# Performance work log

Measured on AMD Instinct MI355X. Metric: run time of the kernel, lower is better.

The kernel has to match this reference:

```python
import jax, jax.numpy as jnp
import numpy as np

N, E, H = 100000, 1250000, 64
NF, EF = 16, 3
BN_EPS = 1e-5
HALF = H // 2


def setup_inputs() -> dict:
    key = jax.random.key(0)
    ks = jax.random.split(key, 24)
    g = lambda i, shape, s=0.05: jax.random.normal(ks[i], shape, dtype=jnp.float32) * s
    return {
        "x": jax.random.normal(ks[0], (N, NF), dtype=jnp.float32),
        "edge_attr": jax.random.normal(ks[1], (E, EF), dtype=jnp.float32),
        "edge_index": jax.random.randint(ks[2], (2, E), 0, N),
        "W_node": g(3, (NF, H)), "b_node": g(4, (H,)),
        "W_edge": g(5, (EF, H)), "b_edge": g(6, (H,)),
        "W_lin0": g(7, (H, H)), "b_lin0": g(8, (H,)),
        "W_att0": g(9, (2 * H + EF, 1)), "b_att0": g(10, (1,)),
        "W_sage_l": g(11, (H, H)), "b_sage_l": g(12, (H,)),
        "W_sage_r": g(13, (H, H)),
        "W_gcn": g(14, (H, H)), "b_gcn": g(15, (H,)),
        "bn_gamma": jnp.ones((3, H), jnp.float32),
        "bn_beta": jnp.zeros((3, H), jnp.float32),
        "W_r1": g(16, (H, H)), "b_r1": g(17, (H,)),
        "W_r2": g(18, (H, HALF)), "b_r2": g(19, (HALF,)),
        "W_r3": g(20, (HALF, 1)), "b_r3": g(21, (1,)),
    }


def _bn_eval(x, gamma, beta):
    # eval-mode BatchNorm1d with running_mean=0, running_var=1
    return x * (gamma / jnp.sqrt(1.0 + BN_EPS)) + beta


def _edge_att(h, src, dst, edge_attr, W, b, Wa, ba):
    # EdgeAttentionLayer: lin -> per-edge attention MLP -> scatter-add at dst
    h = h @ W + b                                   # [N,H]
    hi, hj = h[dst], h[src]                         # [E,H] gathers
    a = jnp.concatenate([hi, hj, edge_attr], -1) @ Wa + ba   # [E,1]
    a = jax.nn.sigmoid(jax.nn.leaky_relu(a, 0.01))
    return jax.ops.segment_sum(hj * a, dst, num_segments=N)


def _sage(h, src, dst, Wl, bl, Wr):
    # SAGEConv (mean aggregation): lin_l(mean_j x_j) + lin_r(x)
    agg = jax.ops.segment_sum(h[src], dst, num_segments=N)
    cnt = jax.ops.segment_sum(jnp.ones((src.shape[0], 1), h.dtype), dst, num_segments=N)
    mean = agg / jnp.maximum(cnt, 1.0)
    return mean @ Wl + bl + h @ Wr


def _gcn(h, src, dst, W, b):
    # GCNConv with self-loops and symmetric normalization
    hw = h @ W
    loop = jnp.arange(N)
    s = jnp.concatenate([src, loop])
    d = jnp.concatenate([dst, loop])
    deg = jax.ops.segment_sum(jnp.ones(s.shape[0], hw.dtype), d, num_segments=N)
    dis = jnp.where(deg > 0, jax.lax.rsqrt(jnp.maximum(deg, 1.0)), 0.0)
    norm = dis[s] * dis[d]                          # [E+N]
    return jax.ops.segment_sum(hw[s] * norm[:, None], d, num_segments=N) + b


def reference(x, edge_attr, edge_index, W_node, b_node, W_edge, b_edge,
              W_lin0, b_lin0, W_att0, b_att0, W_sage_l, b_sage_l, W_sage_r,
              W_gcn, b_gcn, bn_gamma, bn_beta, W_r1, b_r1, W_r2, b_r2, W_r3, b_r3):
    src, dst = edge_index[0], edge_index[1]
    h = x @ W_node + b_node
    _unused = edge_attr @ W_edge + b_edge  # computed in original forward, never used

    # layer 0: EdgeAttentionLayer + BN + ReLU (+residual; eval dropout = identity)
    ident = h
    h = _edge_att(h, src, dst, edge_attr, W_lin0, b_lin0, W_att0, b_att0)
    h = jax.nn.relu(_bn_eval(h, bn_gamma[0], bn_beta[0])) + ident

    # layer 1: SAGEConv
    ident = h
    h = _sage(h, src, dst, W_sage_l, b_sage_l, W_sage_r)
    h = jax.nn.relu(_bn_eval(h, bn_gamma[1], bn_beta[1])) + ident

    # layer 2: GCNConv
    ident = h
    h = _gcn(h, src, dst, W_gcn, b_gcn)
    h = jax.nn.relu(_bn_eval(h, bn_gamma[2], bn_beta[2])) + ident

    h = jax.nn.relu(h @ W_r1 + b_r1)
    h = jax.nn.relu(h @ W_r2 + b_r2)
    return h @ W_r3 + b_r3  # [N,1]
```

## Files before the change

### kernel.cpp

```cpp
#include <hip/hip_runtime.h>
#include <hip/hip_fp16.h>
#include <math.h>

#define NODES 100000
#define EDGES 1250000
#define HD 64
#define NFD 16
#define CHUNK 1024
#define NCHUNK ((NODES + CHUNK - 1) / CHUNK)
#define BN_INV 0.9999950000374996f
#define LP 65


__global__ void k_hist(const int* __restrict__ ei, int* __restrict__ deg) {
  int e = blockIdx.x * blockDim.x + threadIdx.x;
  if (e < EDGES) atomicAdd(&deg[ei[EDGES + e]], 1);
}

__global__ void k_scan1(const int* __restrict__ deg, int* __restrict__ part) {
  __shared__ int lds[256];
  int t = threadIdx.x, b = blockIdx.x;
  int base = b * CHUNK + t * 4;
  int s = 0;
#pragma unroll
  for (int m = 0; m < 4; m++) { int i = base + m; if (i < NODES) s += deg[i]; }
  lds[t] = s; __syncthreads();
  for (int off = 128; off > 0; off >>= 1) {
    if (t < off) lds[t] += lds[t + off];
    __syncthreads();
  }
  if (t == 0) part[b] = lds[0];
}

__global__ void k_scan2(int* __restrict__ part) {
  if (threadIdx.x == 0 && blockIdx.x == 0) {
    int run = 0;
    for (int c = 0; c < NCHUNK; c++) { int v = part[c]; part[c] = run; run += v; }
  }
}

__global__ void k_scan3(const int* __restrict__ deg, const int* __restrict__ part,
                        int* __restrict__ rowptr, int* __restrict__ cur,
                        float* __restrict__ dis) {
  __shared__ int lds[256];
  int t = threadIdx.x, b = blockIdx.x;
  int base = b * CHUNK + t * 4;
  int dl[4]; int s = 0;
#pragma unroll
  for (int m = 0; m < 4; m++) { int i = base + m; dl[m] = (i < NODES) ? deg[i] : 0; s += dl[m]; }
  lds[t] = s; __syncthreads();
  for (int off = 1; off < 256; off <<= 1) {
    int add = (t >= off) ? lds[t - off] : 0;
    __syncthreads();
    lds[t] += add;
    __syncthreads();
  }
  int run = part[b] + lds[t] - s;
#pragma unroll
  for (int m = 0; m < 4; m++) {
    int i = base + m;
    if (i < NODES) {
      rowptr[i] = run; cur[i] = run;
      dis[i] = 1.0f / sqrtf((float)(dl[m] + 1));
    }
    run += dl[m];
  }
  if (b == 0 && t == 0) rowptr[NODES] = EDGES;
}

__global__ void k_fillatt(const int* __restrict__ ei, const float* __restrict__ ea,
                          const float* __restrict__ cvec, const float* __restrict__ dvec,
                          const float* __restrict__ Wa, const float* __restrict__ ba,
                          int* __restrict__ cur, float2* __restrict__ sa) {
  int e = blockIdx.x * blockDim.x + threadIdx.x;
  if (e >= EDGES) return;
  int s = ei[e], d = ei[EDGES + e];
  float alin = cvec[d] + dvec[s] + ea[3 * e] * Wa[128] + ea[3 * e + 1] * Wa[129] +
               ea[3 * e + 2] * Wa[130] + ba[0];
  float lr = alin >= 0.f ? alin : 0.01f * alin;
  float a = 1.f / (1.f + expf(-lr));
  int p = atomicAdd(&cur[d], 1);
  sa[p] = make_float2(__int_as_float(s), a);
}


__device__ __forceinline__ void store16h(__half* dst, const float* v) {
  uint u[8];
#pragma unroll
  for (int j = 0; j < 8; j++) {
    __half2 h = __float22half2_rn(make_float2(v[2 * j], v[2 * j + 1]));
    u[j] = *reinterpret_cast<uint*>(&h);
  }
  uint4* o = (uint4*)dst;
  o[0] = make_uint4(u[0], u[1], u[2], u[3]);
  o[1] = make_uint4(u[4], u[5], u[6], u[7]);
}

#define AGG_BODY16(TABLE, WEXPR0, WEXPR1, WEXPR2, WEXPR3)                        \
  float4 acc0 = make_float4(0.f, 0.f, 0.f, 0.f);                                 \
  float4 acc1 = make_float4(0.f, 0.f, 0.f, 0.f);                                 \
  float4 acc2 = make_float4(0.f, 0.f, 0.f, 0.f);                                 \
  float4 acc3 = make_float4(0.f, 0.f, 0.f, 0.f);                                 \
  int last = end - 1;                                                            \
  for (int m = start; m < end; m += 16) {                                        \
    int e0 = m + sub, e1 = e0 + 4, e2 = e0 + 8, e3 = e0 + 12;                    \
    float2 s0 = sa[min(e0, last)], s1 = sa[min(e1, last)];                       \
    float2 s2 = sa[min(e2, last)], s3 = sa[min(e3, last)];                       \
    float w0 = (e0 < end) ? (WEXPR0) : 0.f;                                      \
    float w1 = (e1 < end) ? (WEXPR1) : 0.f;                                      \
    float w2 = (e2 < end) ? (WEXPR2) : 0.f;                                      \
    float w3 = (e3 < end) ? (WEXPR3) : 0.f;                                      \
    uint2 u0 = *((const uint2*)(TABLE + (size_t)__float_as_int(s0.x) * HD) + col); \
    uint2 u1 = *((const uint2*)(TABLE + (size_t)__float_as_int(s1.x) * HD) + col); \
    uint2 u2 = *((const uint2*)(TABLE + (size_t)__float_as_int(s2.x) * HD) + col); \
    uint2 u3 = *((const uint2*)(TABLE + (size_t)__float_as_int(s3.x) * HD) + col); \
    {                                                                            \
      float2 fa = __half22float2(*reinterpret_cast<__half2*>(&u0.x));            \
      float2 fb = __half22float2(*reinterpret_cast<__half2*>(&u0.y));            \
      acc0.x = fmaf(w0, fa.x, acc0.x); acc0.y = fmaf(w0, fa.y, acc0.y);          \
      acc0.z = fmaf(w0, fb.x, acc0.z); acc0.w = fmaf(w0, fb.y, acc0.w);          \
    }                                                                            \
    {                                                                            \
      float2 fa = __half22float2(*reinterpret_cast<__half2*>(&u1.x));            \
      float2 fb = __half22float2(*reinterpret_cast<__half2*>(&u1.y));            \
      acc1.x = fmaf(w1, fa.x, acc1.x); acc1.y = fmaf(w1, fa.y, acc1.y);          \
      acc1.z = fmaf(w1, fb.x, acc1.z); acc1.w = fmaf(w1, fb.y, acc1.w);          \
    }                                                                            \
    {                                                                            \
      float2 fa = __half22float2(*reinterpret_cast<__half2*>(&u2.x));            \
      float2 fb = __half22float2(*reinterpret_cast<__half2*>(&u2.y));            \
      acc2.x = fmaf(w2, fa.x, acc2.x); acc2.y = fmaf(w2, fa.y, acc2.y);          \
      acc2.z = fmaf(w2, fb.x, acc2.z); acc2.w = fmaf(w2, fb.y, acc2.w);          \
    }                                                                            \
    {                                                                            \
      float2 fa = __half22float2(*reinterpret_cast<__half2*>(&u3.x));            \
      float2 fb = __half22float2(*reinterpret_cast<__half2*>(&u3.y));            \
      acc3.x = fmaf(w3, fa.x, acc3.x); acc3.y = fmaf(w3, fa.y, acc3.y);          \
      acc3.z = fmaf(w3, fb.x, acc3.z); acc3.w = fmaf(w3, fb.y, acc3.w);          \
    }                                                                            \
  }                                                                              \
  acc0.x = (acc0.x + acc1.x) + (acc2.x + acc3.x);                                \
  acc0.y = (acc0.y + acc1.y) + (acc2.y + acc3.y);                                \
  acc0.z = (acc0.z + acc1.z) + (acc2.z + acc3.z);                                \
  acc0.w = (acc0.w + acc1.w) + (acc2.w + acc3.w);                                \
  _Pragma("unroll")                                                              \
  for (int off = 16; off <= 32; off <<= 1) {                                     \
    acc0.x += __shfl_xor(acc0.x, off); acc0.y += __shfl_xor(acc0.y, off);        \
    acc0.z += __shfl_xor(acc0.z, off); acc0.w += __shfl_xor(acc0.w, off);        \
  }


__global__ __launch_bounds__(256) void k_lin0(
    const float* __restrict__ x,
    const float* __restrict__ Wn, const float* __restrict__ bn,
    const float* __restrict__ Wl, const float* __restrict__ bl,
    const float* __restrict__ Wa,
    float* __restrict__ hA, __half* __restrict__ hB16,
    float* __restrict__ cvec, float* __restrict__ dvec) {
  __shared__ float sh[64 * LP];
  __shared__ float sc[4][64], sd[4][64];
  int slot = threadIdx.x & 63;
  int cc = __builtin_amdgcn_readfirstlane(threadIdx.x >> 6);
  int c0 = cc * 16;
  int n0 = blockIdx.x * 64 + slot;
  bool valid = n0 < NODES;
  int n = valid ? n0 : NODES - 1;
  const float4* xr = (const float4*)(x + (size_t)n * NFD);
  float acc[16];
#pragma unroll
  for (int j = 0; j < 16; j++) acc[j] = bn[c0 + j];
#pragma unroll
  for (int q = 0; q < 4; q++) {
    float4 xa = xr[q];
    float xs[4] = {xa.x, xa.y, xa.z, xa.w};
#pragma unroll
    for (int t = 0; t < 4; t++)
#pragma unroll
      for (int j = 0; j < 16; j++)
        acc[j] = fmaf(xs[t], Wn[(q * 4 + t) * HD + c0 + j], acc[j]);
  }
#pragma unroll
  for (int j = 0; j < 16; j++) sh[slot * LP + c0 + j] = acc[j];
  if (valid) {
    float4* o = (float4*)(hA + (size_t)n * HD + c0);
    o[0] = make_float4(acc[0], acc[1], acc[2], acc[3]);
    o[1] = make_float4(acc[4], acc[5], acc[6], acc[7]);
    o[2] = make_float4(acc[8], acc[9], acc[10], acc[11]);
    o[3] = make_float4(acc[12], acc[13], acc[14], acc[15]);
  }
  __syncthreads();
  float a2[16];
#pragma unroll
  for (int j = 0; j < 16; j++) a2[j] = bl[c0 + j];
#pragma unroll 8
  for (int k = 0; k < 64; k++) {
    float hk = sh[slot * LP + k];
#pragma unroll
    for (int j = 0; j < 16; j++)
      a2[j] = fmaf(hk, Wl[k * HD + c0 + j], a2[j]);
  }
  float cn = 0.f, dn = 0.f;
#pragma unroll
  for (int j = 0; j < 16; j++) {
    cn = fmaf(a2[j], Wa[c0 + j], cn);
    dn = fmaf(a2[j], Wa[64 + c0 + j], dn);
  }
  if (valid) store16h(hB16 + (size_t)n * HD + c0, a2);
  sc[cc][slot] = cn;
  sd[cc][slot] = dn;
  __syncthreads();
  if (cc == 0 && valid) {
    cvec[n] = sc[0][slot] + sc[1][slot] + sc[2][slot] + sc[3][slot];
    dvec[n] = sd[0][slot] + sd[1][slot] + sd[2][slot] + sd[3][slot];
  }
}

__global__ __launch_bounds__(256) void k_agg_att(
    const float2* __restrict__ sa, const int* __restrict__ rowptr,
    const float* __restrict__ hA, const __half* __restrict__ hB16,
    const float* __restrict__ g, const float* __restrict__ bt,
    float* __restrict__ hC, __half* __restrict__ hC16) {
  int lane = threadIdx.x & 63;
  int node = __builtin_amdgcn_readfirstlane(blockIdx.x * 4 + (threadIdx.x >> 6));
  if (node >= NODES) return;
  int start = rowptr[node], end = rowptr[node + 1];
  int sub = lane >> 4, col = lane & 15;
  float4 gg = ((const float4*)g)[col];
  float4 bb = ((const float4*)bt)[col];
  float4 ha = *((const float4*)(hA + (size_t)node * HD) + col);
  AGG_BODY16(hB16, s0.y, s1.y, s2.y, s3.y)
  if (lane < 16) {
    float4 v;
    v.x = fmaxf(acc0.x * (gg.x * BN_INV) + bb.x, 0.f) + ha.x;
    v.y = fmaxf(acc0.y * (gg.y * BN_INV) + bb.y, 0.f) + ha.y;
    v.z = fmaxf(acc0.z * (gg.z * BN_INV) + bb.z, 0.f) + ha.z;
    v.w = fmaxf(acc0.w * (gg.w * BN_INV) + bb.w, 0.f) + ha.w;
    *((float4*)(hC + (size_t)node * HD) + col) = v;
    __half2 p0 = __float22half2_rn(make_float2(v.x, v.y));
    __half2 p1 = __float22half2_rn(make_float2(v.z, v.w));
    uint2 u;
    u.x = *reinterpret_cast<uint*>(&p0);
    u.y = *reinterpret_cast<uint*>(&p1);
    *((uint2*)(hC16 + (size_t)node * HD) + col) = u;
  }
}

__global__ __launch_bounds__(256) void k_msage(
    const float2* __restrict__ sa, const int* __restrict__ rowptr,
    const float* __restrict__ hC, const __half* __restrict__ hC16,
    const float* __restrict__ Wl, const float* __restrict__ bl,
    const float* __restrict__ Wr, const float* __restrict__ Wg,
    const float* __restrict__ g, const float* __restrict__ bt,
    const float* __restrict__ dis,
    float* __restrict__ hA, float* __restrict__ hD, __half* __restrict__ hD16) {
  __shared__ float sh[64 * LP];
  int lane = threadIdx.x & 63;
  int wu = __builtin_amdgcn_readfirstlane(threadIdx.x >> 6);
  int sub = lane >> 4, col = lane & 15;
  int nbase = blockIdx.x * 64;
  for (int i = 0; i < 16; i++) {
    int slot = wu * 16 + i;
    int nn = min(nbase + slot, NODES - 1);
    int start = rowptr[nn], end = rowptr[nn + 1];
    float rdeg = 1.f / fmaxf((float)(end - start), 1.f);
    AGG_BODY16(hC16, 1.f, 1.f, 1.f, 1.f)
    if (lane < 16) {
      sh[slot * LP + col * 4 + 0] = acc0.x * rdeg;
      sh[slot * LP + col * 4 + 1] = acc0.y * rdeg;
      sh[slot * LP + col * 4 + 2] = acc0.z * rdeg;
      sh[slot * LP + col * 4 + 3] = acc0.w * rdeg;
    }
  }
  __syncthreads();
  int c0 = wu * 16;
  int n0 = nbase + lane;
  bool valid = n0 < NODES;
  int n = valid ? n0 : NODES - 1;
  const float4* cr = (const float4*)(hC + (size_t)n * HD);
  float acc[16];
#pragma unroll
  for (int j = 0; j < 16; j++) acc[j] = bl[c0 + j];
#pragma unroll 8
  for (int k = 0; k < 64; k++) {
    float mk = sh[lane * LP + k];
#pragma unroll
    for (int j = 0; j < 16; j++)
      acc[j] = fmaf(mk, Wl[k * HD + c0 + j], acc[j]);
  }
#pragma unroll 4
  for (int q = 0; q < 16; q++) {
    float4 ac = cr[q];
    float cs[4] = {ac.x, ac.y, ac.z, ac.w};
#pragma unroll
    for (int t = 0; t < 4; t++)
#pragma unroll
      for (int j = 0; j < 16; j++)
        acc[j] = fmaf(cs[t], Wr[(q * 4 + t) * HD + c0 + j], acc[j]);
  }
  float tv[16];
  {
    float4 r0 = cr[wu * 4 + 0], r1 = cr[wu * 4 + 1], r2 = cr[wu * 4 + 2], r3 = cr[wu * 4 + 3];
    float rv[16] = {r0.x, r0.y, r0.z, r0.w, r1.x, r1.y, r1.z, r1.w,
                    r2.x, r2.y, r2.z, r2.w, r3.x, r3.y, r3.z, r3.w};
#pragma unroll
    for (int j = 0; j < 16; j++)
      tv[j] = fmaxf(acc[j] * (g[c0 + j] * BN_INV) + bt[c0 + j], 0.f) + rv[j];
  }
  __syncthreads();
#pragma unroll
  for (int j = 0; j < 16; j++) sh[lane * LP + c0 + j] = tv[j];
  if (valid) {
    float4* o = (float4*)(hA + (size_t)n * HD + c0);
    o[0] = make_float4(tv[0], tv[1], tv[2], tv[3]);
    o[1] = make_float4(tv[4], tv[5], tv[6], tv[7]);
    o[2] = make_float4(tv[8], tv[9], tv[10], tv[11]);
    o[3] = make_float4(tv[12], tv[13], tv[14], tv[15]);
  }
  __syncthreads();
  float di = dis[n];
  float a2[16];
#pragma unroll
  for (int j = 0; j < 16; j++) a2[j] = 0.f;
#pragma unroll 8
  for (int k = 0; k < 64; k++) {
    float tk = sh[lane * LP + k];
#pragma unroll
    for (int j = 0; j < 16; j++)
      a2[j] = fmaf(tk, Wg[k * HD + c0 + j], a2[j]);
  }
#pragma unroll
  for (int j = 0; j < 16; j++) a2[j] *= di;
  if (valid) {
    float4* o = (float4*)(hD + (size_t)n * HD + c0);
    o[0] = make_float4(a2[0], a2[1], a2[2], a2[3]);
    o[1] = make_float4(a2[4], a2[5], a2[6], a2[7]);
    o[2] = make_float4(a2[8], a2[9], a2[10], a2[11]);
    o[3] = make_float4(a2[12], a2[13], a2[14], a2[15]);
    store16h(hD16 + (size_t)n * HD + c0, a2);
  }
}

__global__ __launch_bounds__(256) void k_gcnreg(
    const float2* __restrict__ sa, const int* __restrict__ rowptr,
    const float* __restrict__ dis,
    const float* __restrict__ hA,
    const float* __restrict__ hD,
    const __half* __restrict__ hD16,
    const float* __restrict__ bg,
    const float* __restrict__ g, const float* __restrict__ bt,
    const float* __restrict__ W1, const float* __restrict__ b1,
    const float* __restrict__ W2, const float* __restrict__ b2,
    const float* __restrict__ W3, const float* __restrict__ b3,
    float* __restrict__ out) {
  __shared__ float sh[64 * LP];
  __shared__ float sred[4][64];
  int lane = threadIdx.x & 63;
  int wu = __builtin_amdgcn_readfirstlane(threadIdx.x >> 6);
  int sub = lane >> 4, col = lane & 15;
  int nbase = blockIdx.x * 64;
  float4 gg = ((const float4*)g)[col];
  float4 bb = ((const float4*)bt)[col];
  float4 bgv = ((const float4*)bg)[col];
  for (int i = 0; i < 16; i++) {
    int slot = wu * 16 + i;
    int nn = min(nbase + slot, NODES - 1);
    int start = rowptr[nn], end = rowptr[nn + 1];
    float di = dis[nn];
    float4 sv = *((const float4*)(hD + (size_t)nn * HD) + col);
    float4 ha = *((const float4*)(hA + (size_t)nn * HD) + col);
    AGG_BODY16(hD16, 1.f, 1.f, 1.f, 1.f)
    if (lane < 16) {
      sh[slot * LP + col * 4 + 0] =
          fmaxf((di * (acc0.x + sv.x) + bgv.x) * (gg.x * BN_INV) + bb.x, 0.f) + ha.x;
      sh[slot * LP + col * 4 + 1] =
          fmaxf((di * (acc0.y + sv.y) + bgv.y) * (gg.y * BN_INV) + bb.y, 0.f) + ha.y;
      sh[slot * LP + col * 4 + 2] =
          fmaxf((di * (acc0.z + sv.z) + bgv.z) * (gg.z * BN_INV) + bb.z, 0.f) + ha.z;
      sh[slot * LP + col * 4 + 3] =
          fmaxf((di * (acc0.w + sv.w) + bgv.w) * (gg.w * BN_INV) + bb.w, 0.f) + ha.w;
    }
  }
  __syncthreads();
  int c0 = wu * 16;
  int n0 = nbase + lane;
  bool valid = n0 < NODES;
  int n = valid ? n0 : NODES - 1;
  float acc[16];
#pragma unroll
  for (int j = 0; j < 16; j++) acc[j] = b1[c0 + j];
#pragma unroll 8
  for (int k = 0; k < 64; k++) {
    float rk = sh[lane * LP + k];
#pragma unroll
    for (int j = 0; j < 16; j++)
      acc[j] = fmaf(rk, W1[k * HD + c0 + j], acc[j]);
  }
  float t1v[16];
#pragma unroll
  for (int j = 0; j < 16; j++) t1v[j] = fmaxf(acc[j], 0.f);
  __syncthreads();
#pragma unroll
  for (int j = 0; j < 16; j++) sh[lane * LP + c0 + j] = t1v[j];
  __syncthreads();
  int d0 = wu * 8;
  float a2[8];
#pragma unroll
  for (int j = 0; j < 8; j++) a2[j] = b2[d0 + j];
#pragma unroll 8
  for (int k = 0; k < 64; k++) {
    float tk = sh[lane * LP + k];
#pragma unroll
    for (int j = 0; j < 8; j++)
      a2[j] = fmaf(tk, W2[k * 32 + d0 + j], a2[j]);
  }
  float part = 0.f;
#pragma unroll
  for (int j = 0; j < 8; j++) part = fmaf(fmaxf(a2[j], 0.f), W3[d0 + j], part);
  sred[wu][lane] = part;
  __syncthreads();
  if (wu == 0 && valid)
    out[n] = sred[0][lane] + sred[1][lane] + sred[2][lane] + sred[3][lane] + b3[0];
}


extern "C" void kernel_launch(void* const* d_in, const int* in_sizes, int n_in,
                              void* d_out, int out_size, void* d_ws, size_t ws_size,
                              hipStream_t stream) {
  const float* x      = (const float*)d_in[0];
  const float* ea     = (const float*)d_in[1];
  const int*   ei     = (const int*)d_in[2];
  const float* W_node = (const float*)d_in[3];
  const float* b_node = (const float*)d_in[4];
  const float* W_lin0 = (const float*)d_in[7];
  const float* b_lin0 = (const float*)d_in[8];
  const float* W_att0 = (const float*)d_in[9];
  const float* b_att0 = (const float*)d_in[10];
  const float* W_sl   = (const float*)d_in[11];
  const float* b_sl   = (const float*)d_in[12];
  const float* W_sr   = (const float*)d_in[13];
  const float* W_gcn  = (const float*)d_in[14];
  const float* b_gcn  = (const float*)d_in[15];
  const float* bn_g   = (const float*)d_in[16];
  const float* bn_b   = (const float*)d_in[17];
  const float* W_r1   = (const float*)d_in[18];
  const float* b_r1   = (const float*)d_in[19];
  const float* W_r2   = (const float*)d_in[20];
  const float* b_r2   = (const float*)d_in[21];
  const float* W_r3   = (const float*)d_in[22];
  const float* b_r3   = (const float*)d_in[23];
  float* out = (float*)d_out;

  char* ws = (char*)d_ws;
  size_t o = 0;
  auto alloc = [&](size_t bytes) -> void* {
    void* p = ws + o;
    o += (bytes + 255) & ~(size_t)255;
    return p;
  };
  int*    deg    = (int*)alloc(NODES * 4);
  int*    rowptr = (int*)alloc((NODES + 1) * 4);
  int*    cur    = (int*)alloc(NODES * 4);
  int*    part   = (int*)alloc(256 * 4);
  float2* sa     = (float2*)alloc((size_t)EDGES * 8);
  float*  hA     = (float*)alloc((size_t)NODES * HD * 4);
  float*  hC     = (float*)alloc((size_t)NODES * HD * 4);
  float*  hD     = (float*)alloc((size_t)NODES * HD * 4);
  __half* hB16   = (__half*)alloc((size_t)NODES * HD * 2);
  __half* hC16   = (__half*)alloc((size_t)NODES * HD * 2);
  __half* hD16   = (__half*)alloc((size_t)NODES * HD * 2);
  float*  cvec   = (float*)alloc(NODES * 4);
  float*  dvec   = (float*)alloc(NODES * 4);
  float*  dis    = (float*)alloc(NODES * 4);
  (void)ws_size; (void)in_sizes; (void)n_in; (void)out_size;

  const int EB  = (EDGES + 255) / 256;
  const int NT  = (NODES + 63) / 64;
  const int NBW = (NODES + 3) / 4;

  hipMemsetAsync(deg, 0, NODES * 4, stream);
  k_hist<<<EB, 256, 0, stream>>>(ei, deg);
  k_scan1<<<NCHUNK, 256, 0, stream>>>(deg, part);
  k_scan2<<<1, 64, 0, stream>>>(part);
  k_scan3<<<NCHUNK, 256, 0, stream>>>(deg, part, rowptr, cur, dis);

  k_lin0<<<NT, 256, 0, stream>>>(x, W_node, b_node, W_lin0, b_lin0, W_att0,
                                 hA, hB16, cvec, dvec);
  k_fillatt<<<EB, 256, 0, stream>>>(ei, ea, cvec, dvec, W_att0, b_att0, cur, sa);
  k_agg_att<<<NBW, 256, 0, stream>>>(sa, rowptr, hA, hB16,
                                     bn_g + 0 * HD, bn_b + 0 * HD, hC, hC16);
  k_msage<<<NT, 256, 0, stream>>>(sa, rowptr, hC, hC16, W_sl, b_sl, W_sr, W_gcn,
                                  bn_g + 1 * HD, bn_b + 1 * HD, dis, hA, hD, hD16);
  k_gcnreg<<<NT, 256, 0, stream>>>(sa, rowptr, dis, hA, hD, hD16, b_gcn,
                                   bn_g + 2 * HD, bn_b + 2 * HD,
                                   W_r1, b_r1, W_r2, b_r2, W_r3, b_r3, out);
}
```

Before: 341.3 us.

## Use 8 waves per block and interleave two-node gathers in SAGE/GCN kernels

The fused SAGE and GCN+regressor kernels go from 256 to 512 threads per block, so each wave aggregates 8 nodes instead of 16 and computes 8 instead of 16 output columns in the dense stages. Inside the aggregation loop each wave now walks two nodes' neighbor lists together, issuing both sets of gathers per iteration to raise memory-level parallelism. The macro body is moved into inline helper functions. The cost is more registers for the paired accumulators and wasted iterations when the two nodes' degrees differ.

Result: slower. 351.7 us (+3.0%).

```diff
diff --git a/kernel.cpp b/kernel.cpp
--- a/kernel.cpp
+++ b/kernel.cpp
@@ -96,58 +96,81 @@
   o[1] = make_uint4(u[4], u[5], u[6], u[7]);
 }
 
-#define AGG_BODY16(TABLE, WEXPR0, WEXPR1, WEXPR2, WEXPR3)                        \
+__device__ __forceinline__ void store8h(__half* dst, const float* v) {
+  uint u[4];
+#pragma unroll
+  for (int j = 0; j < 4; j++) {
+    __half2 h = __float22half2_rn(make_float2(v[2 * j], v[2 * j + 1]));
+    u[j] = *reinterpret_cast<uint*>(&h);
+  }
+  *(uint4*)dst = make_uint4(u[0], u[1], u[2], u[3]);
+}
+
+__device__ __forceinline__ void gstep(const __half* __restrict__ tab,
+                                      const float2* __restrict__ sa,
+                                      int m, int end, int last, int sub, int col,
+                                      bool weighted,
+                                      float4& A0, float4& A1, float4& A2, float4& A3) {
+  int e0 = m + sub, e1 = e0 + 4, e2 = e0 + 8, e3 = e0 + 12;
+  float2 s0 = sa[min(e0, last)], s1 = sa[min(e1, last)];
+  float2 s2 = sa[min(e2, last)], s3 = sa[min(e3, last)];
+  float w0 = (e0 < end) ? (weighted ? s0.y : 1.f) : 0.f;
+  float w1 = (e1 < end) ? (weighted ? s1.y : 1.f) : 0.f;
+  float w2 = (e2 < end) ? (weighted ? s2.y : 1.f) : 0.f;
+  float w3 = (e3 < end) ? (weighted ? s3.y : 1.f) : 0.f;
+  uint2 u0 = *((const uint2*)(tab + (size_t)__float_as_int(s0.x) * HD) + col);
+  uint2 u1 = *((const uint2*)(tab + (size_t)__float_as_int(s1.x) * HD) + col);
+  uint2 u2 = *((const uint2*)(tab + (size_t)__float_as_int(s2.x) * HD) + col);
+  uint2 u3 = *((const uint2*)(tab + (size_t)__float_as_int(s3.x) * HD) + col);
+  {
+    float2 fa = __half22float2(*reinterpret_cast<__half2*>(&u0.x));
+    float2 fb = __half22float2(*reinterpret_cast<__half2*>(&u0.y));
+    A0.x = fmaf(w0, fa.x, A0.x); A0.y = fmaf(w0, fa.y, A0.y);
+    A0.z = fmaf(w0, fb.x, A0.z); A0.w = fmaf(w0, fb.y, A0.w);
+  }
+  {
+    float2 fa = __half22float2(*reinterpret_cast<__half2*>(&u1.x));
+    float2 fb = __half22float2(*reinterpret_cast<__half2*>(&u1.y));
+    A1.x = fmaf(w1, fa.x, A1.x); A1.y = fmaf(w1, fa.y, A1.y);
+    A1.z = fmaf(w1, fb.x, A1.z); A1.w = fmaf(w1, fb.y, A1.w);
+  }
+  {
+    float2 fa = __half22float2(*reinterpret_cast<__half2*>(&u2.x));
+    float2 fb = __half22float2(*reinterpret_cast<__half2*>(&u2.y));
+    A2.x = fmaf(w2, fa.x, A2.x); A2.y = fmaf(w2, fa.y, A2.y);
+    A2.z = fmaf(w2, fb.x, A2.z); A2.w = fmaf(w2, fb.y, A2.w);
+  }
+  {
+    float2 fa = __half22float2(*reinterpret_cast<__half2*>(&u3.x));
+    float2 fb = __half22float2(*reinterpret_cast<__half2*>(&u3.y));
+    A3.x = fmaf(w3, fa.x, A3.x); A3.y = fmaf(w3, fa.y, A3.y);
+    A3.z = fmaf(w3, fb.x, A3.z); A3.w = fmaf(w3, fb.y, A3.w);
+  }
+}
+
+__device__ __forceinline__ float4 red4(float4 a0, float4 a1, float4 a2, float4 a3) {
+  float4 r;
+  r.x = (a0.x + a1.x) + (a2.x + a3.x);
+  r.y = (a0.y + a1.y) + (a2.y + a3.y);
+  r.z = (a0.z + a1.z) + (a2.z + a3.z);
+  r.w = (a0.w + a1.w) + (a2.w + a3.w);
+#pragma unroll
+  for (int off = 16; off <= 32; off <<= 1) {
+    r.x += __shfl_xor(r.x, off); r.y += __shfl_xor(r.y, off);
+    r.z += __shfl_xor(r.z, off); r.w += __shfl_xor(r.w, off);
+  }
+  return r;
+}
+
+#define AGG_BODY16(TABLE, WEIGHTED)                                              \
   float4 acc0 = make_float4(0.f, 0.f, 0.f, 0.f);                                 \
   float4 acc1 = make_float4(0.f, 0.f, 0.f, 0.f);                                 \
   float4 acc2 = make_float4(0.f, 0.f, 0.f, 0.f);                                 \
   float4 acc3 = make_float4(0.f, 0.f, 0.f, 0.f);                                 \
   int last = end - 1;                                                            \
-  for (int m = start; m < end; m += 16) {                                        \
-    int e0 = m + sub, e1 = e0 + 4, e2 = e0 + 8, e3 = e0 + 12;                    \
-    float2 s0 = sa[min(e0, last)], s1 = sa[min(e1, last)];                       \
-    float2 s2 = sa[min(e2, last)], s3 = sa[min(e3, last)];                       \
-    float w0 = (e0 < end) ? (WEXPR0) : 0.f;                                      \
-    float w1 = (e1 < end) ? (WEXPR1) : 0.f;                                      \
-    float w2 = (e2 < end) ? (WEXPR2) : 0.f;                                      \
-    float w3 = (e3 < end) ? (WEXPR3) : 0.f;                                      \
-    uint2 u0 = *((const uint2*)(TABLE + (size_t)__float_as_int(s0.x) * HD) + col); \
-    uint2 u1 = *((const uint2*)(TABLE + (size_t)__float_as_int(s1.x) * HD) + col); \
-    uint2 u2 = *((const uint2*)(TABLE + (size_t)__float_as_int(s2.x) * HD) + col); \
-    uint2 u3 = *((const uint2*)(TABLE + (size_t)__float_as_int(s3.x) * HD) + col); \
-    {                                                                            \
-      float2 fa = __half22float2(*reinterpret_cast<__half2*>(&u0.x));            \
-      float2 fb = __half22float2(*reinterpret_cast<__half2*>(&u0.y));            \
-      acc0.x = fmaf(w0, fa.x, acc0.x); acc0.y = fmaf(w0, fa.y, acc0.y);          \
-      acc0.z = fmaf(w0, fb.x, acc0.z); acc0.w = fmaf(w0, fb.y, acc0.w);          \
-    }                                                                            \
-    {                                                                            \
-      float2 fa = __half22float2(*reinterpret_cast<__half2*>(&u1.x));            \
-      float2 fb = __half22float2(*reinterpret_cast<__half2*>(&u1.y));            \
-      acc1.x = fmaf(w1, fa.x, acc1.x); acc1.y = fmaf(w1, fa.y, acc1.y);          \
-      acc1.z = fmaf(w1, fb.x, acc1.z); acc1.w = fmaf(w1, fb.y, acc1.w);          \
-    }                                                                            \
-    {                                                                            \
-      float2 fa = __half22float2(*reinterpret_cast<__half2*>(&u2.x));            \
-      float2 fb = __half22float2(*reinterpret_cast<__half2*>(&u2.y));            \
-      acc2.x = fmaf(w2, fa.x, acc2.x); acc2.y = fmaf(w2, fa.y, acc2.y);          \
-      acc2.z = fmaf(w2, fb.x, acc2.z); acc2.w = fmaf(w2, fb.y, acc2.w);          \
-    }                                                                            \
-    {                                                                            \
-      float2 fa = __half22float2(*reinterpret_cast<__half2*>(&u3.x));            \
-      float2 fb = __half22float2(*reinterpret_cast<__half2*>(&u3.y));            \
-      acc3.x = fmaf(w3, fa.x, acc3.x); acc3.y = fmaf(w3, fa.y, acc3.y);          \
-      acc3.z = fmaf(w3, fb.x, acc3.z); acc3.w = fmaf(w3, fb.y, acc3.w);          \
-    }                                                                            \
-  }                                                                              \
-  acc0.x = (acc0.x + acc1.x) + (acc2.x + acc3.x);                                \
-  acc0.y = (acc0.y + acc1.y) + (acc2.y + acc3.y);                                \
-  acc0.z = (acc0.z + acc1.z) + (acc2.z + acc3.z);                                \
-  acc0.w = (acc0.w + acc1.w) + (acc2.w + acc3.w);                                \
-  _Pragma("unroll")                                                              \
-  for (int off = 16; off <= 32; off <<= 1) {                                     \
-    acc0.x += __shfl_xor(acc0.x, off); acc0.y += __shfl_xor(acc0.y, off);        \
-    acc0.z += __shfl_xor(acc0.z, off); acc0.w += __shfl_xor(acc0.w, off);        \
-  }
+  for (int m = start; m < end; m += 16)                                          \
+    gstep(TABLE, sa, m, end, last, sub, col, WEIGHTED, acc0, acc1, acc2, acc3);  \
+  float4 accr = red4(acc0, acc1, acc2, acc3);
 
 
 __global__ __launch_bounds__(256) void k_lin0(
@@ -228,13 +251,13 @@
   float4 gg = ((const float4*)g)[col];
   float4 bb = ((const float4*)bt)[col];
   float4 ha = *((const float4*)(hA + (size_t)node * HD) + col);
-  AGG_BODY16(hB16, s0.y, s1.y, s2.y, s3.y)
+  AGG_BODY16(hB16, true)
   if (lane < 16) {
     float4 v;
-    v.x = fmaxf(acc0.x * (gg.x * BN_INV) + bb.x, 0.f) + ha.x;
-    v.y = fmaxf(acc0.y * (gg.y * BN_INV) + bb.y, 0.f) + ha.y;
-    v.z = fmaxf(acc0.z * (gg.z * BN_INV) + bb.z, 0.f) + ha.z;
-    v.w = fmaxf(acc0.w * (gg.w * BN_INV) + bb.w, 0.f) + ha.w;
+    v.x = fmaxf(accr.x * (gg.x * BN_INV) + bb.x, 0.f) + ha.x;
+    v.y = fmaxf(accr.y * (gg.y * BN_INV) + bb.y, 0.f) + ha.y;
+    v.z = fmaxf(accr.z * (gg.z * BN_INV) + bb.z, 0.f) + ha.z;
+    v.w = fmaxf(accr.w * (gg.w * BN_INV) + bb.w, 0.f) + ha.w;
     *((float4*)(hC + (size_t)node * HD) + col) = v;
     __half2 p0 = __float22half2_rn(make_float2(v.x, v.y));
     __half2 p1 = __float22half2_rn(make_float2(v.z, v.w));
@@ -245,7 +268,7 @@
   }
 }
 
-__global__ __launch_bounds__(256) void k_msage(
+__global__ __launch_bounds__(512) void k_msage(
     const float2* __restrict__ sa, const int* __restrict__ rowptr,
     const float* __restrict__ hC, const __half* __restrict__ hC16,
     const float* __restrict__ Wl, const float* __restrict__ bl,
@@ -258,33 +281,52 @@
   int wu = __builtin_amdgcn_readfirstlane(threadIdx.x >> 6);
   int sub = lane >> 4, col = lane & 15;
   int nbase = blockIdx.x * 64;
-  for (int i = 0; i < 16; i++) {
-    int slot = wu * 16 + i;
-    int nn = min(nbase + slot, NODES - 1);
-    int start = rowptr[nn], end = rowptr[nn + 1];
-    float rdeg = 1.f / fmaxf((float)(end - start), 1.f);
-    AGG_BODY16(hC16, 1.f, 1.f, 1.f, 1.f)
+  for (int i = 0; i < 8; i += 2) {
+    int slotA = wu * 8 + i, slotB = slotA + 1;
+    int nA = min(nbase + slotA, NODES - 1);
+    int nB = min(nbase + slotB, NODES - 1);
+    int sA = rowptr[nA], eA = rowptr[nA + 1];
+    int sB = rowptr[nB], eB = rowptr[nB + 1];
+    int lenA = eA - sA, lenB = eB - sB;
+    int lastA = (lenA > 0) ? eA - 1 : 0;
+    int lastB = (lenB > 0) ? eB - 1 : 0;
+    float rdA = 1.f / fmaxf((float)lenA, 1.f);
+    float rdB = 1.f / fmaxf((float)lenB, 1.f);
+    float4 A0 = make_float4(0, 0, 0, 0), A1 = A0, A2 = A0, A3 = A0;
+    float4 B0 = A0, B1 = A0, B2 = A0, B3 = A0;
+    int iters = (max(lenA, lenB) + 15) >> 4;
+    int mA = sA, mB = sB;
+    for (int it = 0; it < iters; ++it, mA += 16, mB += 16) {
+      gstep(hC16, sa, mA, eA, lastA, sub, col, false, A0, A1, A2, A3);
+      gstep(hC16, sa, mB, eB, lastB, sub, col, false, B0, B1, B2, B3);
+    }
+    float4 ra = red4(A0, A1, A2, A3);
+    float4 rb = red4(B0, B1, B2, B3);
     if (lane < 16) {
-      sh[slot * LP + col * 4 + 0] = acc0.x * rdeg;
-      sh[slot * LP + col * 4 + 1] = acc0.y * rdeg;
-      sh[slot * LP + col * 4 + 2] = acc0.z * rdeg;
-      sh[slot * LP + col * 4 + 3] = acc0.w * rdeg;
+      sh[slotA * LP + col * 4 + 0] = ra.x * rdA;
+      sh[slotA * LP + col * 4 + 1] = ra.y * rdA;
+      sh[slotA * LP + col * 4 + 2] = ra.z * rdA;
+      sh[slotA * LP + col * 4 + 3] = ra.w * rdA;
+      sh[slotB * LP + col * 4 + 0] = rb.x * rdB;
+      sh[slotB * LP + col * 4 + 1] = rb.y * rdB;
+      sh[slotB * LP + col * 4 + 2] = rb.z * rdB;
+      sh[slotB * LP + col * 4 + 3] = rb.w * rdB;
     }
   }
   __syncthreads();
-  int c0 = wu * 16;
+  int c0 = wu * 8;
   int n0 = nbase + lane;
   bool valid = n0 < NODES;
   int n = valid ? n0 : NODES - 1;
   const float4* cr = (const float4*)(hC + (size_t)n * HD);
-  float acc[16];
-#pragma unroll
-  for (int j = 0; j < 16; j++) acc[j] = bl[c0 + j];
+  float acc[8];
+#pragma unroll
+  for (int j = 0; j < 8; j++) acc[j] = bl[c0 + j];
 #pragma unroll 8
   for (int k = 0; k < 64; k++) {
     float mk = sh[lane * LP + k];
 #pragma unroll
-    for (int j = 0; j < 16; j++)
+    for (int j = 0; j < 8; j++)
       acc[j] = fmaf(mk, Wl[k * HD + c0 + j], acc[j]);
   }
 #pragma unroll 4
@@ -294,53 +336,48 @@
 #pragma unroll
     for (int t = 0; t < 4; t++)
 #pragma unroll
-      for (int j = 0; j < 16; j++)
+      for (int j = 0; j < 8; j++)
         acc[j] = fmaf(cs[t], Wr[(q * 4 + t) * HD + c0 + j], acc[j]);
   }
-  float tv[16];
+  float tv[8];
   {
-    float4 r0 = cr[wu * 4 + 0], r1 = cr[wu * 4 + 1], r2 = cr[wu * 4 + 2], r3 = cr[wu * 4 + 3];
-    float rv[16] = {r0.x, r0.y, r0.z, r0.w, r1.x, r1.y, r1.z, r1.w,
-                    r2.x, r2.y, r2.z, r2.w, r3.x, r3.y, r3.z, r3.w};
-#pragma unroll
-    for (int j = 0; j < 16; j++)
+    float4 r0 = cr[wu * 2], r1 = cr[wu * 2 + 1];
+    float rv[8] = {r0.x, r0.y, r0.z, r0.w, r1.x, r1.y, r1.z, r1.w};
+#pragma unroll
+    for (int j = 0; j < 8; j++)
       tv[j] = fmaxf(acc[j] * (g[c0 + j] * BN_INV) + bt[c0 + j], 0.f) + rv[j];
   }
   __syncthreads();
 #pragma unroll
-  for (int j = 0; j < 16; j++) sh[lane * LP + c0 + j] = tv[j];
+  for (int j = 0; j < 8; j++) sh[lane * LP + c0 + j] = tv[j];
   if (valid) {
     float4* o = (float4*)(hA + (size_t)n * HD + c0);
     o[0] = make_float4(tv[0], tv[1], tv[2], tv[3]);
     o[1] = make_float4(tv[4], tv[5], tv[6], tv[7]);
-    o[2] = make_float4(tv[8], tv[9], tv[10], tv[11]);
-    o[3] = make_float4(tv[12], tv[13], tv[14], tv[15]);
   }
   __syncthreads();
   float di = dis[n];
-  float a2[16];
-#pragma unroll
-  for (int j = 0; j < 16; j++) a2[j] = 0.f;
+  float a2[8];
+#pragma unroll
+  for (int j = 0; j < 8; j++) a2[j] = 0.f;
 #pragma unroll 8
   for (int k = 0; k < 64; k++) {
     float tk = sh[lane * LP + k];
 #pragma unroll
-    for (int j = 0; j < 16; j++)
+    for (int j = 0; j < 8; j++)
       a2[j] = fmaf(tk, Wg[k * HD + c0 + j], a2[j]);
   }
 #pragma unroll
-  for (int j = 0; j < 16; j++) a2[j] *= di;
+  for (int j = 0; j < 8; j++) a2[j] *= di;
   if (valid) {
     float4* o = (float4*)(hD + (size_t)n * HD + c0);
     o[0] = make_float4(a2[0], a2[1], a2[2], a2[3]);
     o[1] = make_float4(a2[4], a2[5], a2[6], a2[7]);
-    o[2] = make_float4(a2[8], a2[9], a2[10], a2[11]);
-    o[3] = make_float4(a2[12], a2[13], a2[14], a2[15]);
-    store16h(hD16 + (size_t)n * HD + c0, a2);
-  }
-}
-
-__global__ __launch_bounds__(256) void k_gcnreg(
+    store8h(hD16 + (size_t)n * HD + c0, a2);
+  }
+}
+
+__global__ __launch_bounds__(512) void k_gcnreg(
     const float2* __restrict__ sa, const int* __restrict__ rowptr,
     const float* __restrict__ dis,
     const float* __restrict__ hA,
@@ -353,7 +390,7 @@
     const float* __restrict__ W3, const float* __restrict__ b3,
     float* __restrict__ out) {
   __shared__ float sh[64 * LP];
-  __shared__ float sred[4][64];
+  __shared__ float sred[8][64];
   int lane = threadIdx.x & 63;
   int wu = __builtin_amdgcn_readfirstlane(threadIdx.x >> 6);
   int sub = lane >> 4, col = lane & 15;
@@ -361,65 +398,93 @@
   float4 gg = ((const float4*)g)[col];
   float4 bb = ((const float4*)bt)[col];
   float4 bgv = ((const float4*)bg)[col];
-  for (int i = 0; i < 16; i++) {
-    int slot = wu * 16 + i;
-    int nn = min(nbase + slot, NODES - 1);
-    int start = rowptr[nn], end = rowptr[nn + 1];
-    float di = dis[nn];
-    float4 sv = *((const float4*)(hD + (size_t)nn * HD) + col);
-    float4 ha = *((const float4*)(hA + (size_t)nn * HD) + col);
-    AGG_BODY16(hD16, 1.f, 1.f, 1.f, 1.f)
+  for (int i = 0; i < 8; i += 2) {
+    int slotA = wu * 8 + i, slotB = slotA + 1;
+    int nA = min(nbase + slotA, NODES - 1);
+    int nB = min(nbase + slotB, NODES - 1);
+    int sA = rowptr[nA], eA = rowptr[nA + 1];
+    int sB = rowptr[nB], eB = rowptr[nB + 1];
+    int lenA = eA - sA, lenB = eB - sB;
+    int lastA = (lenA > 0) ? eA - 1 : 0;
+    int lastB = (lenB > 0) ? eB - 1 : 0;
+    float diA = dis[nA], diB = dis[nB];
+    float4 svA = *((const float4*)(hD + (size_t)nA * HD) + col);
+    float4 svB = *((const float4*)(hD + (size_t)nB * HD) + col);
+    float4 haA = *((const float4*)(hA + (size_t)nA * HD) + col);
+    float4 haB = *((const float4*)(hA + (size_t)nB * HD) + col);
+    float4 A0 = make_float4(0, 0, 0, 0), A1 = A0, A2 = A0, A3 = A0;
+    float4 B0 = A0, B1 = A0, B2 = A0, B3 = A0;
+    int iters = (max(lenA, lenB) + 15) >> 4;
+    int mA = sA, mB = sB;
+    for (int it = 0; it < iters; ++it, mA += 16, mB += 16) {
+      gstep(hD16, sa, mA, eA, lastA, sub, col, false, A0, A1, A2, A3);
+      gstep(hD16, sa, mB, eB, lastB, sub, col, false, B0, B1, B2, B3);
+    }
+    float4 ra = red4(A0, A1, A2, A3);
+    float4 rb = red4(B0, B1, B2, B3);
     if (lane < 16) {
-      sh[slot * LP + col * 4 + 0] =
-          fmaxf((di * (acc0.x + sv.x) + bgv.x) * (gg.x * BN_INV) + bb.x, 0.f) + ha.x;
-      sh[slot * LP + col * 4 + 1] =
-          fmaxf((di * (acc0.y + sv.y) + bgv.y) * (gg.y * BN_INV) + bb.y, 0.f) + ha.y;
-      sh[slot * LP + col * 4 + 2] =
-          fmaxf((di * (acc0.z + sv.z) + bgv.z) * (gg.z * BN_INV) + bb.z, 0.f) + ha.z;
-      sh[slot * LP + col * 4 + 3] =
-          fmaxf((di * (acc0.w + sv.w) + bgv.w) * (gg.w * BN_INV) + bb.w, 0.f) + ha.w;
+      sh[slotA * LP + col * 4 + 0] =
+          fmaxf((diA * (ra.x + svA.x) + bgv.x) * (gg.x * BN_INV) + bb.x, 0.f) + haA.x;
+      sh[slotA * LP + col * 4 + 1] =
+          fmaxf((diA * (ra.y + svA.y) + bgv.y) * (gg.y * BN_INV) + bb.y, 0.f) + haA.y;
+      sh[slotA * LP + col * 4 + 2] =
+          fmaxf((diA * (ra.z + svA.z) + bgv.z) * (gg.z * BN_INV) + bb.z, 0.f) + haA.z;
+      sh[slotA * LP + col * 4 + 3] =
+          fmaxf((diA * (ra.w + svA.w) + bgv.w) * (gg.w * BN_INV) + bb.w, 0.f) + haA.w;
+      sh[slotB * LP + col * 4 + 0] =
+          fmaxf((diB * (rb.x + svB.x) + bgv.x) * (gg.x * BN_INV) + bb.x, 0.f) + haB.x;
+      sh[slotB * LP + col * 4 + 1] =
+          fmaxf((diB * (rb.y + svB.y) + bgv.y) * (gg.y * BN_INV) + bb.y, 0.f) + haB.y;
+      sh[slotB * LP + col * 4 + 2] =
+          fmaxf((diB * (rb.z + svB.z) + bgv.z) * (gg.z * BN_INV) + bb.z, 0.f) + haB.z;
+      sh[slotB * LP + col * 4 + 3] =
+          fmaxf((diB * (rb.w + svB.w) + bgv.w) * (gg.w * BN_INV) + bb.w, 0.f) + haB.w;
     }
   }
   __syncthreads();
-  int c0 = wu * 16;
+  int c0 = wu * 8;
   int n0 = nbase + lane;
   bool valid = n0 < NODES;
   int n = valid ? n0 : NODES - 1;
-  float acc[16];
-#pragma unroll
-  for (int j = 0; j < 16; j++) acc[j] = b1[c0 + j];
+  float acc[8];
+#pragma unroll
+  for (int j = 0; j < 8; j++) acc[j] = b1[c0 + j];
 #pragma unroll 8
   for (int k = 0; k < 64; k++) {
     float rk = sh[lane * LP + k];
 #pragma unroll
-    for (int j = 0; j < 16; j++)
+    for (int j = 0; j < 8; j++)
       acc[j] = fmaf(rk, W1[k * HD + c0 + j], acc[j]);
   }
-  float t1v[16];
-#pragma unroll
-  for (int j = 0; j < 16; j++) t1v[j] = fmaxf(acc[j], 0.f);
-  __syncthreads();
-#pragma unroll
-  for (int j = 0; j < 16; j++) sh[lane * LP + c0 + j] = t1v[j];
-  __syncthreads();
-  int d0 = wu * 8;
-  float a2[8];
-#pragma unroll
-  for (int j = 0; j < 8; j++) a2[j] = b2[d0 + j];
+  float t1v[8];
+#pragma unroll
+  for (int j = 0; j < 8; j++) t1v[j] = fmaxf(acc[j], 0.f);
+  __syncthreads();
+#pragma unroll
+  for (int j = 0; j < 8; j++) sh[lane * LP + c0 + j] = t1v[j];
+  __syncthreads();
+  int d0 = wu * 4;
+  float a2[4];
+#pragma unroll
+  for (int j = 0; j < 4; j++) a2[j] = b2[d0 + j];
 #pragma unroll 8
   for (int k = 0; k < 64; k++) {
     float tk = sh[lane * LP + k];
 #pragma unroll
-    for (int j = 0; j < 8; j++)
+    for (int j = 0; j < 4; j++)
       a2[j] = fmaf(tk, W2[k * 32 + d0 + j], a2[j]);
   }
   float part = 0.f;
 #pragma unroll
-  for (int j = 0; j < 8; j++) part = fmaf(fmaxf(a2[j], 0.f), W3[d0 + j], part);
+  for (int j = 0; j < 4; j++) part = fmaf(fmaxf(a2[j], 0.f), W3[d0 + j], part);
   sred[wu][lane] = part;
   __syncthreads();
-  if (wu == 0 && valid)
-    out[n] = sred[0][lane] + sred[1][lane] + sred[2][lane] + sred[3][lane] + b3[0];
+  if (wu == 0 && valid) {
+    float s = b3[0];
+#pragma unroll
+    for (int w = 0; w < 8; w++) s += sred[w][lane];
+    out[n] = s;
+  }
 }
 
 
@@ -488,9 +553,9 @@
   k_fillatt<<<EB, 256, 0, stream>>>(ei, ea, cvec, dvec, W_att0, b_att0, cur, sa);
   k_agg_att<<<NBW, 256, 0, stream>>>(sa, rowptr, hA, hB16,
                                      bn_g + 0 * HD, bn_b + 0 * HD, hC, hC16);
-  k_msage<<<NT, 256, 0, stream>>>(sa, rowptr, hC, hC16, W_sl, b_sl, W_sr, W_gcn,
+  k_msage<<<NT, 512, 0, stream>>>(sa, rowptr, hC, hC16, W_sl, b_sl, W_sr, W_gcn,
                                   bn_g + 1 * HD, bn_b + 1 * HD, dis, hA, hD, hD16);
-  k_gcnreg<<<NT, 256, 0, stream>>>(sa, rowptr, dis, hA, hD, hD16, b_gcn,
+  k_gcnreg<<<NT, 512, 0, stream>>>(sa, rowptr, dis, hA, hD, hD16, b_gcn,
                                    bn_g + 2 * HD, bn_b + 2 * HD,
                                    W_r1, b_r1, W_r2, b_r2, W_r3, b_r3, out);
 }
```
